# Performance work log

Hardware: AMD Instinct MI355X
Metric: run time of the kernel (lower is better)

## Reference

```python
import jax, jax.numpy as jnp
import numpy as np

N = 100000
D = 256
E = 3200000


def setup_inputs() -> dict:
    key = jax.random.key(0)
    ks = jax.random.split(key, 8)
    x = jax.random.normal(ks[0], (N, D), dtype=jnp.float32)
    edge_index = jax.random.randint(ks[1], (2, E), 0, N, dtype=jnp.int64)
    s = 1.0 / np.sqrt(D)
    W_l = jax.random.uniform(ks[2], (D, D), dtype=jnp.float32, minval=-s, maxval=s)
    b_l = jax.random.uniform(ks[3], (D,), dtype=jnp.float32, minval=-s, maxval=s)
    W_r = jax.random.uniform(ks[4], (D, D), dtype=jnp.float32, minval=-s, maxval=s)
    ln_gamma = jnp.ones((D,), dtype=jnp.float32)
    ln_beta = jnp.zeros((D,), dtype=jnp.float32)
    return {"x": x, "edge_index": edge_index, "W_l": W_l, "b_l": b_l,
            "W_r": W_r, "ln_gamma": ln_gamma, "ln_beta": ln_beta}


def reference(x, edge_index, W_l, b_l, W_r, ln_gamma, ln_beta):
    src, dst = edge_index[0], edge_index[1]
    n = x.shape[0]
    # mean aggregation of neighbor (source) features onto destination nodes
    msg_sum = jax.ops.segment_sum(x[src], dst, num_segments=n)        # [N, D]
    deg = jax.ops.segment_sum(jnp.ones((src.shape[0],), x.dtype), dst,
                              num_segments=n)                          # [N]
    agg = msg_sum / jnp.maximum(deg, 1.0)[:, None]
    # SAGEConv: lin_l(agg) + lin_r(x)   (bias in lin_l only)
    f = agg @ W_l.T + b_l + x @ W_r.T
    # exact-erf GELU (torch F.gelu default)
    f = jax.nn.gelu(f, approximate=False)
    # LayerNorm over feature dim
    mu = jnp.mean(f, axis=-1, keepdims=True)
    var = jnp.var(f, axis=-1, keepdims=True)
    f = (f - mu) * jax.lax.rsqrt(var + 1e-5) * ln_gamma + ln_beta
    # dropout in eval mode = identity; residual add
    return f + x
```

## Files before the change

### kernel.cpp

```cpp
#include <hip/hip_runtime.h>

#define D 256
#define KDIM 512
#define BCAP 16384
#define EPB 8192
#define BM 64

typedef __bf16 bf16_t;
typedef bf16_t bf16x8 __attribute__((ext_vector_type(8)));
typedef bf16_t bf16x4 __attribute__((ext_vector_type(4)));
typedef float f32x4_t __attribute__((ext_vector_type(4)));
typedef float f32x2_t __attribute__((ext_vector_type(2)));


__global__ __launch_bounds__(256) void k_scatter1(const int* __restrict__ eidx,
                                                  int* __restrict__ bcur,
                                                  int* __restrict__ staging, int E) {
    __shared__ int lhist[512];
    __shared__ int lcur[512];
    __shared__ int gbase[512];
    const int t = threadIdx.x;
    const int e0 = blockIdx.x * EPB;
    int e1 = e0 + EPB;
    if (e1 > E) e1 = E;

    lhist[t] = 0;
    lhist[t + 256] = 0;
    lcur[t] = 0;
    lcur[t + 256] = 0;
    __syncthreads();

    for (int e = e0 + t; e < e1; e += 256) {
        int d = eidx[E + e];
        atomicAdd(&lhist[d >> 8], 1);
    }
    __syncthreads();

#pragma unroll
    for (int b = t; b < 512; b += 256) {
        int c = lhist[b];
        gbase[b] = (c > 0) ? atomicAdd(&bcur[b * 16], c) : 0;
    }
    __syncthreads();

    for (int e = e0 + t; e < e1; e += 256) {
        int s = eidx[e];
        int d = eidx[E + e];
        int b = d >> 8;
        int pos = gbase[b] + atomicAdd(&lcur[b], 1);
        staging[(size_t)b * BCAP + pos] = ((d & 255) << 24) | s;
    }
}

__global__ __launch_bounds__(512) void k_bbase(const int* __restrict__ bcur,
                                               int* __restrict__ bbase,
                                               int* __restrict__ row_ptr,
                                               int B1, int N, int E) {
    __shared__ int sm[512];
    int t = threadIdx.x;
    int v = (t < B1) ? bcur[t * 16] : 0;
    sm[t] = v;
    __syncthreads();
    for (int off = 1; off < 512; off <<= 1) {
        int u = (t >= off) ? sm[t - off] : 0;
        __syncthreads();
        sm[t] += u;
        __syncthreads();
    }
    if (t < B1) bbase[t] = sm[t] - v;
    if (t == 0) row_ptr[N] = E;
}

__global__ __launch_bounds__(256) void k_bucket(const int* __restrict__ bcur,
                                                const int* __restrict__ bbase,
                                                const int* __restrict__ staging,
                                                int* __restrict__ edge_src,
                                                int* __restrict__ row_ptr, int N) {
    __shared__ int lhist[256];
    __shared__ int lscan[256];
    __shared__ int lcur[256];
    int b = blockIdx.x, t = threadIdx.x;
    int node_base = b << 8;
    int nn = N - node_base;
    if (nn > 256) nn = 256;
    int cnt = bcur[b * 16];
    int base = bbase[b];
    const int* stg = staging + (size_t)b * BCAP;

    lhist[t] = 0;
    __syncthreads();
    for (int i = t; i < cnt; i += 256)
        atomicAdd(&lhist[((unsigned)stg[i]) >> 24], 1);
    __syncthreads();
    int v = lhist[t];
    lscan[t] = v;
    __syncthreads();
    for (int off = 1; off < 256; off <<= 1) {
        int u = (t >= off) ? lscan[t - off] : 0;
        __syncthreads();
        lscan[t] += u;
        __syncthreads();
    }
    int excl = lscan[t] - v;
    if (t < nn) row_ptr[node_base + t] = base + excl;
    lscan[t] = excl;
    lcur[t] = 0;
    __syncthreads();
    for (int i = t; i < cnt; i += 256) {
        int w = stg[i];
        int ln = ((unsigned)w) >> 24;
        int src = w & 0xFFFFFF;
        int pos = base + lscan[ln] + atomicAdd(&lcur[ln], 1);
        edge_src[pos] = src;
    }
}


__global__ __launch_bounds__(256) void k_convw(const float* __restrict__ Wl,
                                               const float* __restrict__ Wr,
                                               bf16_t* __restrict__ Wcat2) {
    int i = blockIdx.x * 256 + threadIdx.x;
    if (i >= KDIM * D / 4) return;
    int o = i * 4;
    int j = o >> 8;
    int k = o & 255;
    const float* src = (j < D) ? (Wl + (size_t)j * D + k)
                               : (Wr + (size_t)(j - D) * D + k);
    float4 v = *(const float4*)src;
    bf16x4 ov = {(bf16_t)v.x, (bf16_t)v.y, (bf16_t)v.z, (bf16_t)v.w};
    *(bf16x4*)(Wcat2 + o) = ov;
}


__global__ __launch_bounds__(256) void k_gemm(
        const float* __restrict__ x, const bf16_t* __restrict__ Wcat2,
        const float* __restrict__ b_l, unsigned char* __restrict__ Hq,
        bf16_t* __restrict__ Hr, int M) {
    __shared__ __align__(16) bf16_t A_lds[BM * D];

    const int tid = threadIdx.x;
    const int lane = tid & 63;
    const int wid = tid >> 6;
    const int lr = lane & 15;
    const int lh = lane >> 4;
    const int row0 = blockIdx.x * BM;

#pragma unroll
    for (int o = 0; o < 8; ++o) {
        int idx = o * 256 + tid;
        int r = idx >> 5;
        int j = idx & 31;
        int gr = row0 + r;
        if (gr > M - 1) gr = M - 1;
        int lb = j ^ (r & 7);
        float4 u0 = *(const float4*)(x + (size_t)gr * D + lb * 8);
        float4 u1 = *(const float4*)(x + (size_t)gr * D + lb * 8 + 4);
        bf16x8 v = {(bf16_t)u0.x, (bf16_t)u0.y, (bf16_t)u0.z, (bf16_t)u0.w,
                    (bf16_t)u1.x, (bf16_t)u1.y, (bf16_t)u1.z, (bf16_t)u1.w};
        *(bf16x8*)&A_lds[idx * 8] = v;
    }
    __syncthreads();

    f32x4_t acc[4][4];

#define KLOOP(COLOFF)                                                          \
    _Pragma("unroll") for (int k0 = 0; k0 < 256; k0 += 32) {                   \
        const int kb = (k0 >> 3) + lh;                                         \
        bf16x8 a[4], b[4];                                                     \
        _Pragma("unroll") for (int mt = 0; mt < 4; mt++) {                     \
            int ra = mt * 16 + lr;                                             \
            a[mt] = *(const bf16x8*)&A_lds[ra * D + ((kb ^ (ra & 7)) << 3)];   \
        }                                                                      \
        _Pragma("unroll") for (int nt = 0; nt < 4; nt++) {                     \
            int c = (COLOFF) + wid * 64 + nt * 16 + lr;                        \
            b[nt] = *(const bf16x8*)(Wcat2 + (size_t)c * D + k0 + lh * 8);     \
        }                                                                      \
        _Pragma("unroll") for (int mt = 0; mt < 4; mt++)                       \
            _Pragma("unroll") for (int nt = 0; nt < 4; nt++)                   \
                acc[mt][nt] = __builtin_amdgcn_mfma_f32_16x16x32_bf16(         \
                    a[mt], b[nt], acc[mt][nt], 0, 0, 0);                       \
    }

#pragma unroll
    for (int i = 0; i < 4; i++)
#pragma unroll
        for (int j = 0; j < 4; j++) acc[i][j] = (f32x4_t){0.f, 0.f, 0.f, 0.f};
    KLOOP(0)
#pragma unroll
    for (int mt = 0; mt < 4; mt++) {
#pragma unroll
        for (int r = 0; r < 4; r++) {
            int m = row0 + mt * 16 + lh * 4 + r;
            if (m < M) {
#pragma unroll
                for (int nt = 0; nt < 4; nt++) {
                    int c = wid * 64 + nt * 16 + lr;
                    float u = acc[mt][nt][r];
                    int w = __builtin_amdgcn_cvt_pk_fp8_f32(u, u, 0, false);
                    Hq[(size_t)m * D + c] = (unsigned char)(w & 0xff);
                }
            }
        }
    }

    float bl[4];
#pragma unroll
    for (int nt = 0; nt < 4; nt++) bl[nt] = b_l[wid * 64 + nt * 16 + lr];
#pragma unroll
    for (int i = 0; i < 4; i++)
#pragma unroll
        for (int j = 0; j < 4; j++) acc[i][j] = (f32x4_t){0.f, 0.f, 0.f, 0.f};
    KLOOP(256)
#undef KLOOP
#pragma unroll
    for (int mt = 0; mt < 4; mt++) {
#pragma unroll
        for (int r = 0; r < 4; r++) {
            int m = row0 + mt * 16 + lh * 4 + r;
            if (m < M) {
#pragma unroll
                for (int nt = 0; nt < 4; nt++) {
                    int c = wid * 64 + nt * 16 + lr;
                    Hr[(size_t)m * D + c] = (bf16_t)(acc[mt][nt][r] + bl[nt]);
                }
            }
        }
    }
}


__global__ __launch_bounds__(256) void k_final(
        const int* __restrict__ row_ptr, const int* __restrict__ edge_src,
        const unsigned char* __restrict__ Hq, const bf16_t* __restrict__ Hr,
        const float* __restrict__ x, const float* __restrict__ gamma,
        const float* __restrict__ beta, float* __restrict__ out, int N) {
    int wv = threadIdx.x >> 6;
    int lane = threadIdx.x & 63;
    int node = blockIdx.x * 4 + wv;
    if (node >= N) return;
    int g = lane >> 4;
    int c16 = lane & 15;
    int beg = row_ptr[node];
    int end = row_ptr[node + 1];
    const unsigned int* Hqw = (const unsigned int*)Hq;

    float acc[16];
#pragma unroll
    for (int k = 0; k < 16; k++) acc[k] = 0.f;

#define ACC4(w, bidx)                                            \
    {                                                            \
        f32x2_t lo = __builtin_amdgcn_cvt_pk_f32_fp8((w), false);\
        f32x2_t hi = __builtin_amdgcn_cvt_pk_f32_fp8((w), true); \
        acc[(bidx) + 0] += lo[0];                                \
        acc[(bidx) + 1] += lo[1];                                \
        acc[(bidx) + 2] += hi[0];                                \
        acc[(bidx) + 3] += hi[1];                                \
    }

    for (int j = beg; j < end; j += 8) {
        int j0 = j + g, j1 = j + 4 + g;
        bool ok0 = j0 < end, ok1 = j1 < end;
        int s0 = edge_src[ok0 ? j0 : beg];
        int s1 = edge_src[ok1 ? j1 : beg];
        uint4 v0 = *(const uint4*)(Hqw + (size_t)s0 * 64 + c16 * 4);
        uint4 v1 = *(const uint4*)(Hqw + (size_t)s1 * 64 + c16 * 4);
        if (!ok0) { v0.x = 0; v0.y = 0; v0.z = 0; v0.w = 0; }
        if (!ok1) { v1.x = 0; v1.y = 0; v1.z = 0; v1.w = 0; }
        ACC4(v0.x, 0) ACC4(v0.y, 4) ACC4(v0.z, 8) ACC4(v0.w, 12)
        ACC4(v1.x, 0) ACC4(v1.y, 4) ACC4(v1.z, 8) ACC4(v1.w, 12)
    }
#undef ACC4

#pragma unroll
    for (int k = 0; k < 16; k++) {
        acc[k] += __shfl_xor(acc[k], 16, 64);
        acc[k] += __shfl_xor(acc[k], 32, 64);
    }
    int dg = end - beg;
    float inv = 1.0f / (float)(dg > 0 ? dg : 1);

    int col0 = c16 * 16 + g * 4;
    bf16x4 hr = *(const bf16x4*)(Hr + (size_t)node * D + col0);
    float v[4];
    float s = 0.f, ss = 0.f;
#pragma unroll
    for (int j = 0; j < 4; j++) {
        float t = (g == 0) ? acc[j]
                : (g == 1) ? acc[4 + j]
                : (g == 2) ? acc[8 + j]
                           : acc[12 + j];
        float u = t * inv + (float)hr[j];
        float ge = 0.5f * u * (1.0f + erff(u * 0.70710678118654752f));
        v[j] = ge;
        s += ge;
        ss += ge * ge;
    }
#pragma unroll
    for (int off = 1; off <= 32; off <<= 1) {
        s += __shfl_xor(s, off, 64);
        ss += __shfl_xor(ss, off, 64);
    }
    float mean = s * (1.0f / 256.0f);
    float var = ss * (1.0f / 256.0f) - mean * mean;
    float rstd = rsqrtf(var + 1e-5f);

    float4 ga = *(const float4*)(gamma + col0);
    float4 be = *(const float4*)(beta + col0);
    float4 xr = *(const float4*)(x + (size_t)node * D + col0);
    float4 o;
#pragma unroll
    for (int j = 0; j < 4; j++)
        (&o.x)[j] = (v[j] - mean) * rstd * (&ga.x)[j] + (&be.x)[j] + (&xr.x)[j];
    *(float4*)(out + (size_t)node * D + col0) = o;
}


extern "C" void kernel_launch(void* const* d_in, const int* in_sizes, int n_in,
                              void* d_out, int out_size, void* d_ws, size_t ws_size,
                              hipStream_t stream) {
    const float* x = (const float*)d_in[0];
    const int* eidx = (const int*)d_in[1];
    const float* W_l = (const float*)d_in[2];
    const float* b_l = (const float*)d_in[3];
    const float* W_r = (const float*)d_in[4];
    const float* gamma = (const float*)d_in[5];
    const float* beta = (const float*)d_in[6];
    float* out = (float*)d_out;

    const int N = in_sizes[0] / D;
    const int E = in_sizes[1] / 2;
    const int B1 = (N + 255) >> 8;

    char* basep = (char*)d_ws;
    size_t off = 0;
    auto take = [&](size_t bytes) -> void* {
        void* r = basep + off;
        off += (bytes + 255) & ~(size_t)255;
        return r;
    };
    bf16_t* Hr = (bf16_t*)take((size_t)N * D * sizeof(bf16_t));
    unsigned char* Hq = (unsigned char*)take((size_t)N * D);
    int* edge_src = (int*)take((size_t)E * sizeof(int));
    bf16_t* Wcat2 = (bf16_t*)take((size_t)KDIM * D * sizeof(bf16_t));
    int* row_ptr = (int*)take((size_t)(N + 1) * sizeof(int));
    int* bcur = (int*)take((size_t)B1 * 16 * sizeof(int));
    int* bbase = (int*)take((size_t)B1 * sizeof(int));
    int* staging = (int*)Hr;

    hipMemsetAsync(bcur, 0, (size_t)B1 * 16 * sizeof(int), stream);

    k_scatter1<<<(E + EPB - 1) / EPB, 256, 0, stream>>>(eidx, bcur, staging, E);
    k_bbase<<<1, 512, 0, stream>>>(bcur, bbase, row_ptr, B1, N, E);
    k_bucket<<<B1, 256, 0, stream>>>(bcur, bbase, staging, edge_src, row_ptr, N);

    k_convw<<<(KDIM * D / 4 + 255) / 256, 256, 0, stream>>>(W_l, W_r, Wcat2);

    k_gemm<<<(N + BM - 1) / BM, 256, 0, stream>>>(x, Wcat2, b_l, Hq, Hr, N);

    k_final<<<(N + 3) / 4, 256, 0, stream>>>(row_ptr, edge_src, Hq, Hr, x,
                                             gamma, beta, out, N);
}
```

Baseline: 326.8 us.

## Co-schedule CSR build with GEMM halves in merged kernels; split final gather loop

The edge scatter and bucket phases are merged into combined kernels that also run half of the GEMM tiles each, so the latency-bound CSR construction overlaps with compute-bound GEMM blocks. Staging gets its own workspace buffer instead of aliasing Hr, since the GEMM now writes Hr concurrently. The final gather loop gets a mask-free main path for full 8-edge chunks plus a tail, and uses packed float2 accumulators. The merged kernels share a 32KB LDS allocation sized for the GEMM, which may lower occupancy for the scatter and bucket blocks, and the extra staging buffer adds workspace use.

```diff
diff --git a/kernel.cpp b/kernel.cpp
--- a/kernel.cpp
+++ b/kernel.cpp
@@ -13,14 +13,15 @@
 typedef float f32x2_t __attribute__((ext_vector_type(2)));
 
 
-__global__ __launch_bounds__(256) void k_scatter1(const int* __restrict__ eidx,
-                                                  int* __restrict__ bcur,
-                                                  int* __restrict__ staging, int E) {
-    __shared__ int lhist[512];
-    __shared__ int lcur[512];
-    __shared__ int gbase[512];
+__device__ __forceinline__ void scatter_body(int bid, const int* __restrict__ eidx,
+                                             int* __restrict__ bcur,
+                                             int* __restrict__ staging, int E,
+                                             char* smem) {
+    int* lhist = (int*)smem;
+    int* lcur = lhist + 512;
+    int* gbase = lcur + 512;
     const int t = threadIdx.x;
-    const int e0 = blockIdx.x * EPB;
+    const int e0 = bid * EPB;
     int e1 = e0 + EPB;
     if (e1 > E) e1 = E;
 
@@ -52,34 +53,16 @@
     }
 }
 
-__global__ __launch_bounds__(512) void k_bbase(const int* __restrict__ bcur,
-                                               int* __restrict__ bbase,
-                                               int* __restrict__ row_ptr,
-                                               int B1, int N, int E) {
-    __shared__ int sm[512];
+__device__ __forceinline__ void bucket_body(int b, const int* __restrict__ bcur,
+                                            const int* __restrict__ bbase,
+                                            const int* __restrict__ staging,
+                                            int* __restrict__ edge_src,
+                                            int* __restrict__ row_ptr, int N,
+                                            char* smem) {
+    int* lhist = (int*)smem;
+    int* lscan = lhist + 256;
+    int* lcur = lscan + 256;
     int t = threadIdx.x;
-    int v = (t < B1) ? bcur[t * 16] : 0;
-    sm[t] = v;
-    __syncthreads();
-    for (int off = 1; off < 512; off <<= 1) {
-        int u = (t >= off) ? sm[t - off] : 0;
-        __syncthreads();
-        sm[t] += u;
-        __syncthreads();
-    }
-    if (t < B1) bbase[t] = sm[t] - v;
-    if (t == 0) row_ptr[N] = E;
-}
-
-__global__ __launch_bounds__(256) void k_bucket(const int* __restrict__ bcur,
-                                                const int* __restrict__ bbase,
-                                                const int* __restrict__ staging,
-                                                int* __restrict__ edge_src,
-                                                int* __restrict__ row_ptr, int N) {
-    __shared__ int lhist[256];
-    __shared__ int lscan[256];
-    __shared__ int lcur[256];
-    int b = blockIdx.x, t = threadIdx.x;
     int node_base = b << 8;
     int nn = N - node_base;
     if (nn > 256) nn = 256;
@@ -115,35 +98,20 @@
     }
 }
 
-
-__global__ __launch_bounds__(256) void k_convw(const float* __restrict__ Wl,
-                                               const float* __restrict__ Wr,
-                                               bf16_t* __restrict__ Wcat2) {
-    int i = blockIdx.x * 256 + threadIdx.x;
-    if (i >= KDIM * D / 4) return;
-    int o = i * 4;
-    int j = o >> 8;
-    int k = o & 255;
-    const float* src = (j < D) ? (Wl + (size_t)j * D + k)
-                               : (Wr + (size_t)(j - D) * D + k);
-    float4 v = *(const float4*)src;
-    bf16x4 ov = {(bf16_t)v.x, (bf16_t)v.y, (bf16_t)v.z, (bf16_t)v.w};
-    *(bf16x4*)(Wcat2 + o) = ov;
-}
-
-
-__global__ __launch_bounds__(256) void k_gemm(
-        const float* __restrict__ x, const bf16_t* __restrict__ Wcat2,
-        const float* __restrict__ b_l, unsigned char* __restrict__ Hq,
-        bf16_t* __restrict__ Hr, int M) {
-    __shared__ __align__(16) bf16_t A_lds[BM * D];
+__device__ __forceinline__ void gemm_body(int bid, const float* __restrict__ x,
+                                          const bf16_t* __restrict__ Wcat2,
+                                          const float* __restrict__ b_l,
+                                          unsigned char* __restrict__ Hq,
+                                          bf16_t* __restrict__ Hr, int M,
+                                          char* smem) {
+    bf16_t* A_lds = (bf16_t*)smem;
 
     const int tid = threadIdx.x;
     const int lane = tid & 63;
     const int wid = tid >> 6;
     const int lr = lane & 15;
     const int lh = lane >> 4;
-    const int row0 = blockIdx.x * BM;
+    const int row0 = bid * BM;
 
 #pragma unroll
     for (int o = 0; o < 8; ++o) {
@@ -229,6 +197,78 @@
 }
 
 
+__global__ __launch_bounds__(256) void k_sg(const int* __restrict__ eidx,
+                                            int* __restrict__ bcur,
+                                            int* __restrict__ staging, int E,
+                                            const float* __restrict__ x,
+                                            const bf16_t* __restrict__ Wcat2,
+                                            const float* __restrict__ b_l,
+                                            unsigned char* __restrict__ Hq,
+                                            bf16_t* __restrict__ Hr, int M,
+                                            int nScatter) {
+    __shared__ __align__(16) char smem[BM * D * sizeof(bf16_t)];
+    int b = blockIdx.x;
+    if (b < nScatter)
+        scatter_body(b, eidx, bcur, staging, E, smem);
+    else
+        gemm_body(b - nScatter, x, Wcat2, b_l, Hq, Hr, M, smem);
+}
+
+__global__ __launch_bounds__(256) void k_bg(const int* __restrict__ bcur,
+                                            const int* __restrict__ bbase,
+                                            const int* __restrict__ staging,
+                                            int* __restrict__ edge_src,
+                                            int* __restrict__ row_ptr, int N,
+                                            const float* __restrict__ x,
+                                            const bf16_t* __restrict__ Wcat2,
+                                            const float* __restrict__ b_l,
+                                            unsigned char* __restrict__ Hq,
+                                            bf16_t* __restrict__ Hr,
+                                            int B1, int gemmOff) {
+    __shared__ __align__(16) char smem[BM * D * sizeof(bf16_t)];
+    int b = blockIdx.x;
+    if (b < B1)
+        bucket_body(b, bcur, bbase, staging, edge_src, row_ptr, N, smem);
+    else
+        gemm_body(b - B1 + gemmOff, x, Wcat2, b_l, Hq, Hr, N, smem);
+}
+
+__global__ __launch_bounds__(512) void k_bbase(const int* __restrict__ bcur,
+                                               int* __restrict__ bbase,
+                                               int* __restrict__ row_ptr,
+                                               int B1, int N, int E) {
+    __shared__ int sm[512];
+    int t = threadIdx.x;
+    int v = (t < B1) ? bcur[t * 16] : 0;
+    sm[t] = v;
+    __syncthreads();
+    for (int off = 1; off < 512; off <<= 1) {
+        int u = (t >= off) ? sm[t - off] : 0;
+        __syncthreads();
+        sm[t] += u;
+        __syncthreads();
+    }
+    if (t < B1) bbase[t] = sm[t] - v;
+    if (t == 0) row_ptr[N] = E;
+}
+
+
+__global__ __launch_bounds__(256) void k_convw(const float* __restrict__ Wl,
+                                               const float* __restrict__ Wr,
+                                               bf16_t* __restrict__ Wcat2) {
+    int i = blockIdx.x * 256 + threadIdx.x;
+    if (i >= KDIM * D / 4) return;
+    int o = i * 4;
+    int j = o >> 8;
+    int k = o & 255;
+    const float* src = (j < D) ? (Wl + (size_t)j * D + k)
+                               : (Wr + (size_t)(j - D) * D + k);
+    float4 v = *(const float4*)src;
+    bf16x4 ov = {(bf16_t)v.x, (bf16_t)v.y, (bf16_t)v.z, (bf16_t)v.w};
+    *(bf16x4*)(Wcat2 + o) = ov;
+}
+
+
 __global__ __launch_bounds__(256) void k_final(
         const int* __restrict__ row_ptr, const int* __restrict__ edge_src,
         const unsigned char* __restrict__ Hq, const bf16_t* __restrict__ Hr,
@@ -242,40 +282,48 @@
     int c16 = lane & 15;
     int beg = row_ptr[node];
     int end = row_ptr[node + 1];
-    const unsigned int* Hqw = (const unsigned int*)Hq;
-
-    float acc[16];
-#pragma unroll
-    for (int k = 0; k < 16; k++) acc[k] = 0.f;
-
-#define ACC4(w, bidx)                                            \
-    {                                                            \
-        f32x2_t lo = __builtin_amdgcn_cvt_pk_f32_fp8((w), false);\
-        f32x2_t hi = __builtin_amdgcn_cvt_pk_f32_fp8((w), true); \
-        acc[(bidx) + 0] += lo[0];                                \
-        acc[(bidx) + 1] += lo[1];                                \
-        acc[(bidx) + 2] += hi[0];                                \
-        acc[(bidx) + 3] += hi[1];                                \
-    }
-
-    for (int j = beg; j < end; j += 8) {
+    const uint4* hb = (const uint4*)Hq;
+
+    f32x2_t acc2[8];
+#pragma unroll
+    for (int k = 0; k < 8; k++) acc2[k] = (f32x2_t){0.f, 0.f};
+
+#define ACC4(w, i)                                                \
+    {                                                             \
+        acc2[i] += __builtin_amdgcn_cvt_pk_f32_fp8((w), false);   \
+        acc2[(i) + 1] += __builtin_amdgcn_cvt_pk_f32_fp8((w), true); \
+    }
+
+    int j = beg;
+    for (; j + 8 <= end; j += 8) {
+        int s0 = edge_src[j + g];
+        int s1 = edge_src[j + 4 + g];
+        uint4 v0 = hb[(s0 << 4) + c16];
+        uint4 v1 = hb[(s1 << 4) + c16];
+        ACC4(v0.x, 0) ACC4(v0.y, 2) ACC4(v0.z, 4) ACC4(v0.w, 6)
+        ACC4(v1.x, 0) ACC4(v1.y, 2) ACC4(v1.z, 4) ACC4(v1.w, 6)
+    }
+    if (j < end) {
         int j0 = j + g, j1 = j + 4 + g;
         bool ok0 = j0 < end, ok1 = j1 < end;
         int s0 = edge_src[ok0 ? j0 : beg];
         int s1 = edge_src[ok1 ? j1 : beg];
-        uint4 v0 = *(const uint4*)(Hqw + (size_t)s0 * 64 + c16 * 4);
-        uint4 v1 = *(const uint4*)(Hqw + (size_t)s1 * 64 + c16 * 4);
+        uint4 v0 = hb[(s0 << 4) + c16];
+        uint4 v1 = hb[(s1 << 4) + c16];
         if (!ok0) { v0.x = 0; v0.y = 0; v0.z = 0; v0.w = 0; }
         if (!ok1) { v1.x = 0; v1.y = 0; v1.z = 0; v1.w = 0; }
-        ACC4(v0.x, 0) ACC4(v0.y, 4) ACC4(v0.z, 8) ACC4(v0.w, 12)
-        ACC4(v1.x, 0) ACC4(v1.y, 4) ACC4(v1.z, 8) ACC4(v1.w, 12)
+        ACC4(v0.x, 0) ACC4(v0.y, 2) ACC4(v0.z, 4) ACC4(v0.w, 6)
+        ACC4(v1.x, 0) ACC4(v1.y, 2) ACC4(v1.z, 4) ACC4(v1.w, 6)
     }
 #undef ACC4
 
+    float accf[16];
+#pragma unroll
+    for (int k = 0; k < 16; k++) accf[k] = acc2[k >> 1][k & 1];
 #pragma unroll
     for (int k = 0; k < 16; k++) {
-        acc[k] += __shfl_xor(acc[k], 16, 64);
-        acc[k] += __shfl_xor(acc[k], 32, 64);
+        accf[k] += __shfl_xor(accf[k], 16, 64);
+        accf[k] += __shfl_xor(accf[k], 32, 64);
     }
     int dg = end - beg;
     float inv = 1.0f / (float)(dg > 0 ? dg : 1);
@@ -285,14 +333,14 @@
     float v[4];
     float s = 0.f, ss = 0.f;
 #pragma unroll
-    for (int j = 0; j < 4; j++) {
-        float t = (g == 0) ? acc[j]
-                : (g == 1) ? acc[4 + j]
-                : (g == 2) ? acc[8 + j]
-                           : acc[12 + j];
-        float u = t * inv + (float)hr[j];
+    for (int j2 = 0; j2 < 4; j2++) {
+        float t = (g == 0) ? accf[j2]
+                : (g == 1) ? accf[4 + j2]
+                : (g == 2) ? accf[8 + j2]
+                           : accf[12 + j2];
+        float u = t * inv + (float)hr[j2];
         float ge = 0.5f * u * (1.0f + erff(u * 0.70710678118654752f));
-        v[j] = ge;
+        v[j2] = ge;
         s += ge;
         ss += ge * ge;
     }
@@ -310,8 +358,9 @@
     float4 xr = *(const float4*)(x + (size_t)node * D + col0);
     float4 o;
 #pragma unroll
-    for (int j = 0; j < 4; j++)
-        (&o.x)[j] = (v[j] - mean) * rstd * (&ga.x)[j] + (&be.x)[j] + (&xr.x)[j];
+    for (int j2 = 0; j2 < 4; j2++)
+        (&o.x)[j2] = (v[j2] - mean) * rstd * (&ga.x)[j2] + (&be.x)[j2] +
+                     (&xr.x)[j2];
     *(float4*)(out + (size_t)node * D + col0) = o;
 }
 
@@ -331,6 +380,9 @@
     const int N = in_sizes[0] / D;
     const int E = in_sizes[1] / 2;
     const int B1 = (N + 255) >> 8;
+    const int SB = (E + EPB - 1) / EPB;
+    const int GB = (N + BM - 1) / BM;
+    const int GB1 = (GB + 1) / 2;
 
     char* basep = (char*)d_ws;
     size_t off = 0;
@@ -341,22 +393,23 @@
     };
     bf16_t* Hr = (bf16_t*)take((size_t)N * D * sizeof(bf16_t));
     unsigned char* Hq = (unsigned char*)take((size_t)N * D);
+    int* staging = (int*)take((size_t)B1 * BCAP * sizeof(int));
     int* edge_src = (int*)take((size_t)E * sizeof(int));
     bf16_t* Wcat2 = (bf16_t*)take((size_t)KDIM * D * sizeof(bf16_t));
     int* row_ptr = (int*)take((size_t)(N + 1) * sizeof(int));
     int* bcur = (int*)take((size_t)B1 * 16 * sizeof(int));
     int* bbase = (int*)take((size_t)B1 * sizeof(int));
-    int* staging = (int*)Hr;
 
     hipMemsetAsync(bcur, 0, (size_t)B1 * 16 * sizeof(int), stream);
 
-    k_scatter1<<<(E + EPB - 1) / EPB, 256, 0, stream>>>(eidx, bcur, staging, E);
+    k_convw<<<(KDIM * D / 4 + 255) / 256, 256, 0, stream>>>(W_l, W_r, Wcat2);
+
+    k_sg<<<SB + GB1, 256, 0, stream>>>(eidx, bcur, staging, E, x, Wcat2, b_l,
+                                       Hq, Hr, N, SB);
     k_bbase<<<1, 512, 0, stream>>>(bcur, bbase, row_ptr, B1, N, E);
-    k_bucket<<<B1, 256, 0, stream>>>(bcur, bbase, staging, edge_src, row_ptr, N);
-
-    k_convw<<<(KDIM * D / 4 + 255) / 256, 256, 0, stream>>>(W_l, W_r, Wcat2);
-
-    k_gemm<<<(N + BM - 1) / BM, 256, 0, stream>>>(x, Wcat2, b_l, Hq, Hr, N);
+    k_bg<<<B1 + (GB - GB1), 256, 0, stream>>>(bcur, bbase, staging, edge_src,
+                                              row_ptr, N, x, Wcat2, b_l, Hq,
+                                              Hr, B1, GB1);
 
     k_final<<<(N + 3) / 4, 256, 0, stream>>>(row_ptr, edge_src, Hq, Hr, x,
                                              gamma, beta, out, N);
```

Measured after the change: 328.7 us. Within noise of the previous version (+0.6%).
